# Performance work log

Measured on AMD Instinct MI355X. Metric: run time of the kernel, lower is better.

The kernel has to match this reference:

```python
import jax, jax.numpy as jnp
import numpy as np

NUM_HEADS = 16

def setup_inputs() -> dict:
    key = jax.random.key(0)
    ks = jax.random.split(key, 7)
    b, sq, sk, d = 2, 2048, 2048, 1024
    return {
        "query": jax.random.normal(ks[0], (b, sq, d), dtype=jnp.float32),
        "key": jax.random.normal(ks[1], (b, sk, d), dtype=jnp.float32),
        "value": jax.random.normal(ks[2], (b, sk, d), dtype=jnp.float32),
        "key_mask": jax.random.randint(ks[3], (b, sk, 1), 0, 2, dtype=jnp.int32),
        "query_mask": jax.random.randint(ks[4], (b, sq, 1), 0, 2, dtype=jnp.int32),
        "Wo": jax.random.normal(ks[5], (d, d), dtype=jnp.float32) * 0.02,
        "bo": jnp.zeros((d,), dtype=jnp.float32),
    }

def reference(query, key, value, key_mask, query_mask, Wo, bo):
    b, s_q, d = query.shape
    s_k = key.shape[1]
    h = NUM_HEADS
    hd = d // h
    q = query.reshape(b, s_q, h, hd).transpose(0, 2, 1, 3)   # [b,h,sq,hd]
    k = key.reshape(b, s_k, h, hd).transpose(0, 2, 1, 3)     # [b,h,sk,hd]
    v = value.reshape(b, s_k, h, hd).transpose(0, 2, 1, 3)   # [b,h,sk,hd]
    scores = jnp.einsum('bhqd,bhkd->bhqk', q, k) / jnp.sqrt(jnp.float32(hd))
    # dual masking: key_mask [b,sk,1] -> [b,1,1,sk]; query_mask [b,sq,1] -> [b,1,sq,1]
    km = (key_mask[:, :, 0] != 0)[:, None, None, :]
    qm = (query_mask[:, :, 0] != 0)[:, None, :, None]
    valid = km & qm                                           # [b,1,sq,sk]
    scores = jnp.where(valid, scores, -jnp.inf)
    # safe softmax: fully-masked rows -> softmax over zeros, then zeroed out
    # (matches torch: softmax over all -inf gives NaN, nan_to_num -> 0.0)
    row_valid = jnp.any(valid, axis=-1, keepdims=True)        # [b,1,sq,1]
    safe_scores = jnp.where(row_valid, scores, 0.0)
    w = jax.nn.softmax(safe_scores, axis=-1)
    w = jnp.where(row_valid, w, 0.0)
    # dropout is identity (eval mode / p=0)
    out = jnp.einsum('bhqk,bhkd->bhqd', w, v)                 # [b,h,sq,hd]
    out = out.transpose(0, 2, 1, 3).reshape(b, s_q, d)
    return out @ Wo.T + bo
```

## Files before the change

kernel.cpp:

```cpp
#include <hip/hip_runtime.h>

typedef __bf16 bfv8 __attribute__((ext_vector_type(8)));
typedef float f32x4 __attribute__((ext_vector_type(4)));
typedef short s16x8 __attribute__((ext_vector_type(8)));
typedef unsigned int u32;
typedef unsigned int u32x4 __attribute__((ext_vector_type(4)));

#define MFMA16(a,b,c) __builtin_amdgcn_mfma_f32_16x16x32_bf16((a),(b),(c),0,0,0)

__device__ __forceinline__ u32 pk2(float a, float b){
  u32 r; asm("v_cvt_pk_bf16_f32 %0, %1, %2" : "=v"(r) : "v"(a), "v"(b)); return r;
}
__device__ __forceinline__ bfv8 cvt8s(const float* p, float s){
  u32x4 r;
  #pragma unroll
  for (int j=0;j<4;++j) r[j] = pk2(p[2*j]*s, p[2*j+1]*s);
  return *(bfv8*)&r;
}
__device__ __forceinline__ void glds16(const short* g, short* l){
  __builtin_amdgcn_global_load_lds(
      (const __attribute__((address_space(1))) u32*)g,
      (__attribute__((address_space(3))) u32*)l, 16, 0, 0);
}

__global__ __launch_bounds__(256) void prep(const float* __restrict__ K, const float* __restrict__ V,
                                            const float* __restrict__ Wo, const int* __restrict__ km,
                                            short* __restrict__ Kt, short* __restrict__ Vt,
                                            short* __restrict__ Wb, short* __restrict__ kms){
  __shared__ short tl[64][65];
  const int bid = blockIdx.x, tid = threadIdx.x;
  if (bid < 2048){
    int idx = bid*256 + tid;
    int cs = idx & 7, r = (idx >> 3) & 63, kt = (idx >> 9) & 31, bh = idx >> 14;
    int b = bh >> 4, h = bh & 15;
    int c = cs ^ (r & 7);
    const float* src = K + ((size_t)(b*2048 + kt*64 + r))*1024 + h*64 + c*8;
    float4 a = ((const float4*)src)[0], bb = ((const float4*)src)[1];
    u32x4 o;
    o[0]=pk2(a.x,a.y); o[1]=pk2(a.z,a.w); o[2]=pk2(bb.x,bb.y); o[3]=pk2(bb.z,bb.w);
    ((u32x4*)Kt)[idx] = o;
  } else if (bid < 3072){
    int vb = bid - 2048;
    int kt = vb & 31, bh = vb >> 5;
    int b = bh >> 4, h = bh & 15;
    {
      int s = tid >> 2, d0 = (tid & 3) * 16;
      float kmv = (km[b*2048 + kt*64 + s] != 0) ? 1.0f : 0.0f;
      const float* src = V + ((size_t)(b*2048 + kt*64 + s))*1024 + h*64 + d0;
      #pragma unroll
      for (int j = 0; j < 4; ++j){
        float4 v = ((const float4*)src)[j];
        tl[d0+4*j+0][s] = (short)(pk2(v.x*kmv, 0.f) & 0xffff);
        tl[d0+4*j+1][s] = (short)(pk2(v.y*kmv, 0.f) & 0xffff);
        tl[d0+4*j+2][s] = (short)(pk2(v.z*kmv, 0.f) & 0xffff);
        tl[d0+4*j+3][s] = (short)(pk2(v.w*kmv, 0.f) & 0xffff);
      }
    }
    __syncthreads();
    {
      int r = tid >> 2, cp = (tid & 3) * 2;
      short* dst = Vt + (((size_t)(bh*32 + kt)*64 + r) << 6);
      #pragma unroll
      for (int q = 0; q < 2; ++q){
        int cs = cp + q;
        int c = cs ^ (r & 7);
        s16x8 o;
        #pragma unroll
        for (int j = 0; j < 8; ++j){
          int s = c*8 + j;
          int sg = s >> 2, rr = s & 3;
          int t = (sg >> 3)*2 + (sg & 1);
          int a = (sg >> 1) & 3;
          int kap = t*16 + a*4 + rr;
          o[j] = tl[r][kap];
        }
        *(s16x8*)(dst + cs*8) = o;
      }
    }
  } else if (bid < 3584){
    int i = (bid - 3072)*256 + tid;
    const float* p = Wo + (size_t)i*8;
    u32x4 o;
    o[0]=pk2(p[0],p[1]); o[1]=pk2(p[2],p[3]); o[2]=pk2(p[4],p[5]); o[3]=pk2(p[6],p[7]);
    ((u32x4*)Wb)[i] = o;
  } else {
    int i = (bid - 3584)*256 + tid;
    if (i < 4096){
      int bb = i >> 11, kt = (i >> 6) & 31, s = i & 63;
      int rr = s & 3, a = (s >> 3) & 3, t = ((s >> 5) & 1)*2 + ((s >> 2) & 1);
      int key = t*16 + a*4 + rr;
      kms[i] = (km[bb*2048 + kt*64 + key] != 0) ? (short)0x3F80 : (short)0;
    }
  }
}

__global__ __launch_bounds__(512, 4) void attn8(const short* __restrict__ Kt, const short* __restrict__ Vt,
                                                const float* __restrict__ Qf, const short* __restrict__ kms,
                                                const int* __restrict__ qmask, short* __restrict__ X){
  __shared__ __align__(16) short kl[4][64][64];
  __shared__ __align__(16) short vl[4][64][64];
  __shared__ __align__(16) short kml[32][64];
  const int wid = blockIdx.x;
  const int bh = (wid & 7)*4 + (wid >> 7);
  const int qt = (wid >> 3) & 15;
  const int b = bh >> 4, h = bh & 15;
  const int tid = threadIdx.x;
  const int w = tid >> 6, lane = tid & 63, lo = lane & 15, hi = lane >> 4;
  const int toff = (wid * 7) & 31;

  const f32x4 ZERO4 = {0.f, 0.f, 0.f, 0.f};
  const float QSCALE = 0.125f * 1.44269504088896f;
  const int qrow = qt*128 + w*16 + lo;
  bfv8 qf0, qf1;
  {
    const float* qp = Qf + ((size_t)(b*2048 + qrow))*1024 + h*64 + hi*8;
    qf0 = cvt8s(qp, QSCALE);
    qf1 = cvt8s(qp + 32, QSCALE);
  }

  if (w < 4) glds16(kms + b*2048 + w*512 + lane*8, &kml[0][0] + w*512);
  asm volatile("s_waitcnt vmcnt(0)" ::: "memory");
  __builtin_amdgcn_s_barrier();
  __builtin_amdgcn_sched_barrier(0);

  const short* ktb = Kt + ((size_t)(bh*32) << 12);
  const short* vtb = Vt + ((size_t)(bh*32) << 12);

  const int sgoff = w*512 + lane*8;
  const int csK   = (hi ^ (lo & 7)) * 8;

  f32x4 acc[4];
  #pragma unroll
  for (int t2=0;t2<4;++t2) acc[t2] = ZERO4;
  f32x4 accL = ZERO4;

  #pragma unroll
  for (int p = 0; p < 3; ++p){
    const int tp = (toff + p) & 31;
    glds16(ktb + ((size_t)tp << 12) + sgoff, &kl[p][0][0] + w*512);
    asm volatile("" ::: "memory");
    glds16(vtb + ((size_t)tp << 12) + sgoff, &vl[p][0][0] + w*512);
    asm volatile("" ::: "memory");
  }

  for (int i = 0; i < 32; ++i){
    asm volatile("s_waitcnt vmcnt(4)" ::: "memory");
    __builtin_amdgcn_s_barrier();
    __builtin_amdgcn_sched_barrier(0);
    {
      const int tn = (toff + i + 3) & 31, bn = (i + 3) & 3;
      glds16(ktb + ((size_t)tn << 12) + sgoff, &kl[bn][0][0] + w*512);
      asm volatile("" ::: "memory");
      glds16(vtb + ((size_t)tn << 12) + sgoff, &vl[bn][0][0] + w*512);
      asm volatile("" ::: "memory");
    }
    const short (*kc)[64] = kl[i & 3];
    const short (*vc)[64] = vl[i & 3];
    const int tcur = (toff + i) & 31;
    const short* kmrow = &kml[tcur][0];
    bfv8 kmf0 = *(const bfv8*)(kmrow + hi*8);
    bfv8 kmf1 = *(const bfv8*)(kmrow + 32 + hi*8);

    u32 pk[8];
    __builtin_amdgcn_s_setprio(1);
    #pragma unroll
    for (int t=0;t<4;++t){
      const short* rowp = &kc[t*16+lo][0];
      bfv8 kf0 = *(const bfv8*)(rowp + csK);
      bfv8 kf1 = *(const bfv8*)(rowp + (csK ^ 32));
      f32x4 c = MFMA16(kf0, qf0, ZERO4);
      c = MFMA16(kf1, qf1, c);
      float p0 = __builtin_amdgcn_exp2f(c[0]);
      float p1 = __builtin_amdgcn_exp2f(c[1]);
      float p2 = __builtin_amdgcn_exp2f(c[2]);
      float p3 = __builtin_amdgcn_exp2f(c[3]);
      pk[2*t]   = pk2(p0, p1);
      pk[2*t+1] = pk2(p2, p3);
    }
    __builtin_amdgcn_s_setprio(0);
    u32x4 pw0 = {pk[0],pk[1],pk[2],pk[3]};
    u32x4 pw1 = {pk[4],pk[5],pk[6],pk[7]};
    bfv8 pb0 = *(bfv8*)&pw0, pb1 = *(bfv8*)&pw1;

    __builtin_amdgcn_s_setprio(1);
    accL = MFMA16(kmf0, pb0, accL);
    accL = MFMA16(kmf1, pb1, accL);
    #pragma unroll
    for (int t2=0;t2<4;++t2){
      const short* rowp = &vc[t2*16+lo][0];
      bfv8 vf0 = *(const bfv8*)(rowp + csK);
      bfv8 vf1 = *(const bfv8*)(rowp + (csK ^ 32));
      acc[t2] = MFMA16(vf0, pb0, acc[t2]);
      acc[t2] = MFMA16(vf1, pb1, acc[t2]);
    }
    __builtin_amdgcn_s_setprio(0);
  }
  asm volatile("s_waitcnt vmcnt(0)" ::: "memory");

  float l = accL[0];
  float inv = (l > 0.f) ? 1.0f/l : 0.f;
  if (qmask[b*2048 + qrow] == 0) inv = 0.f;
  u32* xp = (u32*)(X + ((size_t)(b*2048 + qrow))*1024 + h*64);
  #pragma unroll
  for (int t2=0;t2<4;++t2){
    xp[t2*8 + 2*hi]     = pk2(acc[t2][0]*inv, acc[t2][1]*inv);
    xp[t2*8 + 2*hi + 1] = pk2(acc[t2][2]*inv, acc[t2][3]*inv);
  }
}

__global__ __launch_bounds__(256) void proj2(const short* __restrict__ X, const short* __restrict__ Wb,
                                             const float* __restrict__ bo, float* __restrict__ Y){
  __shared__ __align__(16) short xl[4][128][32];
  __shared__ __align__(16) short wl[4][64][32];
  const int bid = blockIdx.x;
  const int xcd = bid & 7, ii = bid >> 3;
  const int by = xcd*4 + (ii >> 4);
  const int bx = ii & 15;
  const int tid = threadIdx.x;
  const int w = tid >> 6, lane = tid & 63, lo = lane & 15, hi = lane >> 4;
  const int wr = w >> 1, wc = w & 1;
  const int brow = by*128, bcol = bx*64;
  const f32x4 ZERO4 = {0.f, 0.f, 0.f, 0.f};

  const int cx0 = (w*2+0)*64 + lane, cx1 = (w*2+1)*64 + lane, cw0 = w*64 + lane;
  const int rx0 = cx0 >> 2, rx1 = cx1 >> 2, rw0 = cw0 >> 2;
  const short* xs0 = X  + (size_t)(brow + rx0)*1024 + ((cx0 & 3) ^ (rx0 & 3))*8;
  const short* xs1 = X  + (size_t)(brow + rx1)*1024 + ((cx1 & 3) ^ (rx1 & 3))*8;
  const short* ws0 = Wb + (size_t)(bcol + rw0)*1024 + ((cw0 & 3) ^ (rw0 & 3))*8;

  const int csA = (hi ^ (lo & 3)) * 8;

  f32x4 acc[4][2];
  #pragma unroll
  for (int i=0;i<4;++i){ acc[i][0] = ZERO4; acc[i][1] = ZERO4; }

  #pragma unroll
  for (int p = 0; p < 3; ++p){
    glds16(xs0 + p*32, &xl[p][0][0] + (w*2+0)*512);
    asm volatile("" ::: "memory");
    glds16(xs1 + p*32, &xl[p][0][0] + (w*2+1)*512);
    asm volatile("" ::: "memory");
    glds16(ws0 + p*32, &wl[p][0][0] + w*512);
    asm volatile("" ::: "memory");
  }

  for (int kt = 0; kt < 32; ++kt){
    asm volatile("s_waitcnt vmcnt(6)" ::: "memory");
    __builtin_amdgcn_s_barrier();
    __builtin_amdgcn_sched_barrier(0);
    {
      const int tn = (kt + 3) & 31, bn = (kt + 3) & 3;
      glds16(xs0 + tn*32, &xl[bn][0][0] + (w*2+0)*512);
      asm volatile("" ::: "memory");
      glds16(xs1 + tn*32, &xl[bn][0][0] + (w*2+1)*512);
      asm volatile("" ::: "memory");
      glds16(ws0 + tn*32, &wl[bn][0][0] + w*512);
      asm volatile("" ::: "memory");
    }
    const short* xc = &xl[kt & 3][0][0];
    const short* wcp = &wl[kt & 3][0][0];
    bfv8 a[4], bb[2];
    #pragma unroll
    for (int i=0;i<4;++i) a[i]  = *(const bfv8*)(xc  + (wr*64 + i*16 + lo)*32 + csA);
    #pragma unroll
    for (int j=0;j<2;++j) bb[j] = *(const bfv8*)(wcp + (wc*32 + j*16 + lo)*32 + csA);
    __builtin_amdgcn_s_setprio(1);
    #pragma unroll
    for (int i=0;i<4;++i){
      acc[i][0] = MFMA16(a[i], bb[0], acc[i][0]);
      acc[i][1] = MFMA16(a[i], bb[1], acc[i][1]);
    }
    __builtin_amdgcn_s_setprio(0);
  }
  asm volatile("s_waitcnt vmcnt(0)" ::: "memory");

  float bv[2];
  bv[0] = bo[bcol + wc*32 + lo];
  bv[1] = bo[bcol + wc*32 + 16 + lo];
  #pragma unroll
  for (int i=0;i<4;++i){
    #pragma unroll
    for (int r=0;r<4;++r){
      size_t row = (size_t)(brow + wr*64 + i*16 + hi*4 + r);
      float* yp = Y + row*1024 + bcol + wc*32 + lo;
      yp[0]  = acc[i][0][r] + bv[0];
      yp[16] = acc[i][1][r] + bv[1];
    }
  }
}

extern "C" void kernel_launch(void* const* d_in, const int* in_sizes, int n_in,
                              void* d_out, int out_size, void* d_ws, size_t ws_size,
                              hipStream_t stream){
  const float* Q   = (const float*)d_in[0];
  const float* K   = (const float*)d_in[1];
  const float* V   = (const float*)d_in[2];
  const int* key_mask   = (const int*)d_in[3];
  const int* query_mask = (const int*)d_in[4];
  const float* Wo  = (const float*)d_in[5];
  const float* bo  = (const float*)d_in[6];

  short* Ktw = (short*)d_ws;
  short* Vtw = Ktw + 4194304;
  short* Wb  = Vtw + 4194304;
  short* Xb  = Wb + 1048576;
  short* kms = Xb + 4194304;

  prep<<<3600,256,0,stream>>>(K, V, Wo, key_mask, Ktw, Vtw, Wb, kms);
  attn8<<<512,512,0,stream>>>(Ktw, Vtw, Q, kms, query_mask, Xb);
  proj2<<<512,256,0,stream>>>(Xb, Wb, bo, (float*)d_out);
}
```

Baseline: 78.31 us.

## Process two query sub-tiles per wave to reuse K/V LDS fragments

Each wave now handles 32 query rows (two 16-row groups) instead of 16, so the block covers 256 queries and the grid is halved to 256 blocks. Each K and V fragment read from LDS feeds two MFMAs, halving the K/V global traffic and LDS reads per unit of work. The cost is roughly doubled accumulator and probability registers (occupancy hint lowered to 2) and only 256 blocks on a 256-CU device, which means one wave of blocks with less latency hiding.

```diff
diff --git a/kernel.cpp b/kernel.cpp
--- a/kernel.cpp
+++ b/kernel.cpp
@@ -94,15 +94,15 @@
   }
 }
 
-__global__ __launch_bounds__(512, 4) void attn8(const short* __restrict__ Kt, const short* __restrict__ Vt,
-                                                const float* __restrict__ Qf, const short* __restrict__ kms,
-                                                const int* __restrict__ qmask, short* __restrict__ X){
+__global__ __launch_bounds__(512, 2) void attn10(const short* __restrict__ Kt, const short* __restrict__ Vt,
+                                                 const float* __restrict__ Qf, const short* __restrict__ kms,
+                                                 const int* __restrict__ qmask, short* __restrict__ X){
   __shared__ __align__(16) short kl[4][64][64];
   __shared__ __align__(16) short vl[4][64][64];
   __shared__ __align__(16) short kml[32][64];
   const int wid = blockIdx.x;
-  const int bh = (wid & 7)*4 + (wid >> 7);
-  const int qt = (wid >> 3) & 15;
+  const int bh = (wid & 7)*4 + (wid >> 6);
+  const int qt = (wid >> 3) & 7;
   const int b = bh >> 4, h = bh & 15;
   const int tid = threadIdx.x;
   const int w = tid >> 6, lane = tid & 63, lo = lane & 15, hi = lane >> 4;
@@ -110,12 +110,13 @@
 
   const f32x4 ZERO4 = {0.f, 0.f, 0.f, 0.f};
   const float QSCALE = 0.125f * 1.44269504088896f;
-  const int qrow = qt*128 + w*16 + lo;
-  bfv8 qf0, qf1;
+  const int qrowA = qt*256 + w*32 + lo;
+  const int qrowB = qrowA + 16;
+  bfv8 qa0, qa1, qb0, qb1;
   {
-    const float* qp = Qf + ((size_t)(b*2048 + qrow))*1024 + h*64 + hi*8;
-    qf0 = cvt8s(qp, QSCALE);
-    qf1 = cvt8s(qp + 32, QSCALE);
+    const float* qp = Qf + ((size_t)(b*2048 + qrowA))*1024 + h*64 + hi*8;
+    qa0 = cvt8s(qp, QSCALE);         qa1 = cvt8s(qp + 32, QSCALE);
+    qb0 = cvt8s(qp + 16384, QSCALE); qb1 = cvt8s(qp + 16416, QSCALE);
   }
 
   if (w < 4) glds16(kms + b*2048 + w*512 + lane*8, &kml[0][0] + w*512);
@@ -125,14 +126,13 @@
 
   const short* ktb = Kt + ((size_t)(bh*32) << 12);
   const short* vtb = Vt + ((size_t)(bh*32) << 12);
-
   const int sgoff = w*512 + lane*8;
   const int csK   = (hi ^ (lo & 7)) * 8;
 
-  f32x4 acc[4];
-  #pragma unroll
-  for (int t2=0;t2<4;++t2) acc[t2] = ZERO4;
-  f32x4 accL = ZERO4;
+  f32x4 accA[4], accB[4];
+  #pragma unroll
+  for (int t2=0;t2<4;++t2){ accA[t2] = ZERO4; accB[t2] = ZERO4; }
+  f32x4 accLa = ZERO4, accLb = ZERO4;
 
   #pragma unroll
   for (int p = 0; p < 3; ++p){
@@ -161,50 +161,68 @@
     bfv8 kmf0 = *(const bfv8*)(kmrow + hi*8);
     bfv8 kmf1 = *(const bfv8*)(kmrow + 32 + hi*8);
 
-    u32 pk[8];
+    u32 pka[8], pkb[8];
     __builtin_amdgcn_s_setprio(1);
     #pragma unroll
     for (int t=0;t<4;++t){
       const short* rowp = &kc[t*16+lo][0];
       bfv8 kf0 = *(const bfv8*)(rowp + csK);
       bfv8 kf1 = *(const bfv8*)(rowp + (csK ^ 32));
-      f32x4 c = MFMA16(kf0, qf0, ZERO4);
-      c = MFMA16(kf1, qf1, c);
-      float p0 = __builtin_amdgcn_exp2f(c[0]);
-      float p1 = __builtin_amdgcn_exp2f(c[1]);
-      float p2 = __builtin_amdgcn_exp2f(c[2]);
-      float p3 = __builtin_amdgcn_exp2f(c[3]);
-      pk[2*t]   = pk2(p0, p1);
-      pk[2*t+1] = pk2(p2, p3);
+      f32x4 ca = MFMA16(kf0, qa0, ZERO4);
+      ca = MFMA16(kf1, qa1, ca);
+      f32x4 cb = MFMA16(kf0, qb0, ZERO4);
+      cb = MFMA16(kf1, qb1, cb);
+      float a0 = __builtin_amdgcn_exp2f(ca[0]);
+      float a1 = __builtin_amdgcn_exp2f(ca[1]);
+      float a2 = __builtin_amdgcn_exp2f(ca[2]);
+      float a3 = __builtin_amdgcn_exp2f(ca[3]);
+      float b0 = __builtin_amdgcn_exp2f(cb[0]);
+      float b1 = __builtin_amdgcn_exp2f(cb[1]);
+      float b2 = __builtin_amdgcn_exp2f(cb[2]);
+      float b3 = __builtin_amdgcn_exp2f(cb[3]);
+      pka[2*t]   = pk2(a0, a1); pka[2*t+1] = pk2(a2, a3);
+      pkb[2*t]   = pk2(b0, b1); pkb[2*t+1] = pk2(b2, b3);
     }
     __builtin_amdgcn_s_setprio(0);
-    u32x4 pw0 = {pk[0],pk[1],pk[2],pk[3]};
-    u32x4 pw1 = {pk[4],pk[5],pk[6],pk[7]};
-    bfv8 pb0 = *(bfv8*)&pw0, pb1 = *(bfv8*)&pw1;
+    u32x4 pwa0 = {pka[0],pka[1],pka[2],pka[3]};
+    u32x4 pwa1 = {pka[4],pka[5],pka[6],pka[7]};
+    u32x4 pwb0 = {pkb[0],pkb[1],pkb[2],pkb[3]};
+    u32x4 pwb1 = {pkb[4],pkb[5],pkb[6],pkb[7]};
+    bfv8 pa0 = *(bfv8*)&pwa0, pa1 = *(bfv8*)&pwa1;
+    bfv8 pb0 = *(bfv8*)&pwb0, pb1 = *(bfv8*)&pwb1;
 
     __builtin_amdgcn_s_setprio(1);
-    accL = MFMA16(kmf0, pb0, accL);
-    accL = MFMA16(kmf1, pb1, accL);
+    accLa = MFMA16(kmf0, pa0, accLa);
+    accLa = MFMA16(kmf1, pa1, accLa);
+    accLb = MFMA16(kmf0, pb0, accLb);
+    accLb = MFMA16(kmf1, pb1, accLb);
     #pragma unroll
     for (int t2=0;t2<4;++t2){
       const short* rowp = &vc[t2*16+lo][0];
       bfv8 vf0 = *(const bfv8*)(rowp + csK);
       bfv8 vf1 = *(const bfv8*)(rowp + (csK ^ 32));
-      acc[t2] = MFMA16(vf0, pb0, acc[t2]);
-      acc[t2] = MFMA16(vf1, pb1, acc[t2]);
+      accA[t2] = MFMA16(vf0, pa0, accA[t2]);
+      accA[t2] = MFMA16(vf1, pa1, accA[t2]);
+      accB[t2] = MFMA16(vf0, pb0, accB[t2]);
+      accB[t2] = MFMA16(vf1, pb1, accB[t2]);
     }
     __builtin_amdgcn_s_setprio(0);
   }
   asm volatile("s_waitcnt vmcnt(0)" ::: "memory");
 
-  float l = accL[0];
-  float inv = (l > 0.f) ? 1.0f/l : 0.f;
-  if (qmask[b*2048 + qrow] == 0) inv = 0.f;
-  u32* xp = (u32*)(X + ((size_t)(b*2048 + qrow))*1024 + h*64);
+  float la = accLa[0], lb = accLb[0];
+  float invA = (la > 0.f) ? 1.0f/la : 0.f;
+  float invB = (lb > 0.f) ? 1.0f/lb : 0.f;
+  if (qmask[b*2048 + qrowA] == 0) invA = 0.f;
+  if (qmask[b*2048 + qrowB] == 0) invB = 0.f;
+  u32* xpA = (u32*)(X + ((size_t)(b*2048 + qrowA))*1024 + h*64);
+  u32* xpB = (u32*)(X + ((size_t)(b*2048 + qrowB))*1024 + h*64);
   #pragma unroll
   for (int t2=0;t2<4;++t2){
-    xp[t2*8 + 2*hi]     = pk2(acc[t2][0]*inv, acc[t2][1]*inv);
-    xp[t2*8 + 2*hi + 1] = pk2(acc[t2][2]*inv, acc[t2][3]*inv);
+    xpA[t2*8 + 2*hi]     = pk2(accA[t2][0]*invA, accA[t2][1]*invA);
+    xpA[t2*8 + 2*hi + 1] = pk2(accA[t2][2]*invA, accA[t2][3]*invA);
+    xpB[t2*8 + 2*hi]     = pk2(accB[t2][0]*invB, accB[t2][1]*invB);
+    xpB[t2*8 + 2*hi + 1] = pk2(accB[t2][2]*invB, accB[t2][3]*invB);
   }
 }
 
@@ -307,6 +325,6 @@
   short* kms = Xb + 4194304;
 
   prep<<<3600,256,0,stream>>>(K, V, Wo, key_mask, Ktw, Vtw, Wb, kms);
-  attn8<<<512,512,0,stream>>>(Ktw, Vtw, Q, kms, query_mask, Xb);
+  attn10<<<256,512,0,stream>>>(Ktw, Vtw, Q, kms, query_mask, Xb);
   proj2<<<512,256,0,stream>>>(Xb, Wb, bo, (float*)d_out);
 }
```

After: 78.86 us. Within noise of the previous version (+0.7%).
